# Kernel optimization log

Measured on AMD Instinct MI355X. Metric: run time of the kernel, lower is better.

Reference implementation:

```python
import jax, jax.numpy as jnp
import numpy as np
from jax import lax

DF = 64        # forcing_size: number of teacher-forced latent dims
TF_ALPHA = 0.2 # generalized teacher forcing interpolation weight


def setup_inputs() -> dict:
    key = jax.random.key(0)
    ks = jax.random.split(key, 8)
    B, T, dx, dz, dh, S = 256, 1024, 64, 256, 1024, 16
    x_gt = jax.random.normal(ks[0], (B, T, dx), dtype=jnp.float32)
    subject = jax.random.randint(ks[1], (B,), 0, S, dtype=jnp.int32)
    obs_matrix = jax.random.normal(ks[2], (dz, dx), dtype=jnp.float32) * 0.1
    A_table = jax.random.uniform(ks[3], (S, dz), dtype=jnp.float32) * 0.9
    W1_table = jax.random.normal(ks[4], (S, dz, dh), dtype=jnp.float32) * 0.02
    W2_table = jax.random.normal(ks[5], (S, dh, dz), dtype=jnp.float32) * 0.02
    h1_table = jax.random.normal(ks[6], (S, dz), dtype=jnp.float32) * 0.02
    h2_table = jax.random.normal(ks[7], (S, dh), dtype=jnp.float32) * 0.02
    return {"x_gt": x_gt, "subject": subject, "obs_matrix": obs_matrix,
            "A_table": A_table, "W1_table": W1_table, "W2_table": W2_table,
            "h1_table": h1_table, "h2_table": h2_table}


def reference(x_gt, subject, obs_matrix, A_table, W1_table, W2_table, h1_table, h2_table):
    B, T, dx = x_gt.shape
    dz = obs_matrix.shape[0]
    # encode: x @ pinv(obs_matrix) -> (B, T, dz)
    forcing = x_gt @ jnp.linalg.pinv(obs_matrix)
    # gather per-sample parameters by subject id
    A = A_table[subject]    # (B, dz)
    W1 = W1_table[subject]  # (B, dz, dh)
    W2 = W2_table[subject]  # (B, dh, dz)
    h1 = h1_table[subject]  # (B, dz)
    h2 = h2_table[subject]  # (B, dh)

    z0 = jnp.zeros((B, dz), dtype=x_gt.dtype)
    z0 = z0.at[:, :DF].set(forcing[:, 0, :DF])

    def step(z, f_t):
        # generalized teacher forcing on first DF dims
        z = z.at[:, :DF].set(TF_ALPHA * f_t[:, :DF] + (1.0 - TF_ALPHA) * z[:, :DF])
        # vanilla shPLRNN step: A*z + W1 @ relu(W2 @ z + h2) + h1
        hidden = jax.nn.relu(jnp.einsum('bhz,bz->bh', W2, z) + h2)
        z = A * z + jnp.einsum('bzh,bh->bz', W1, hidden) + h1
        return z, z

    _, Z = lax.scan(step, z0, jnp.transpose(forcing, (1, 0, 2)))  # Z: (T, B, dz)
    # decode: (B, T, dz) @ (dz, dx)
    return jnp.transpose(Z, (1, 0, 2)) @ obs_matrix
```

## Files before the change

kernel.cpp:

```cpp
#include <hip/hip_runtime.h>


typedef _Float16 f16;
typedef _Float16 f16x8 __attribute__((ext_vector_type(8)));
typedef float f32x4 __attribute__((ext_vector_type(4)));

#define TSTEPS 1024

#define WS_C     0ul
#define WS_ZG    16384ul
#define WS_HIDG  802816ul
#define WS_ORDER 2375680ul
#define WS_CNT   2376704ul
#define WS_OFFS  2376768ul
#define WS_CTR   2376832ul
#define WS_XCC   2378880ul
#define WS_NEED  2379392ul

#define SM_ZPK   0
#define SM_ZPRE  26880
#define SM_ZSL   33792
#define SM_TBUF  39936
#define SM_AH    53760
#define SM_ORD   54016
#define SM_SIZE  54208

__device__ __forceinline__ unsigned pack2f16(float x, float y) {
    union { f16 h[2]; unsigned u; } v;
    v.h[0] = (f16)x; v.h[1] = (f16)y;
    return v.u;
}

__device__ __forceinline__ void group_barrier(int* ctr, int target, bool light) {
    __syncthreads();
    if (threadIdx.x == 0) {
        if (!light)
            __builtin_amdgcn_fence(__ATOMIC_RELEASE, "agent");
        __hip_atomic_fetch_add(ctr, 1, __ATOMIC_RELAXED, __HIP_MEMORY_SCOPE_AGENT);
        while (__hip_atomic_load(ctr, __ATOMIC_RELAXED, __HIP_MEMORY_SCOPE_AGENT) < target)
            __builtin_amdgcn_s_sleep(1);
        if (!light)
            __builtin_amdgcn_fence(__ATOMIC_ACQUIRE, "agent");
        else
            asm volatile("buffer_inv" ::: "memory");
    }
    __syncthreads();
}

__global__ __launch_bounds__(256) void prep_kernel(const float* __restrict__ M,
                                                   float* __restrict__ C) {
    __shared__ float aug[64 * 132];
    __shared__ float fac[64];
    int tid = threadIdx.x;
    {
        int i = tid >> 2;
        int j0 = (tid & 3) * 16;
        float acc[16];
        #pragma unroll
        for (int e = 0; e < 16; ++e) acc[e] = 0.f;
        for (int r = 0; r < 256; ++r) {
            float mi = M[r*64 + i];
            #pragma unroll
            for (int e = 0; e < 16; ++e) acc[e] += mi * M[r*64 + j0 + e];
        }
        #pragma unroll
        for (int e = 0; e < 16; ++e) aug[i*132 + j0 + e] = acc[e];
    }
    for (int idx = tid; idx < 4096; idx += 256) {
        int x = idx >> 6, c = idx & 63;
        aug[x*132 + 64 + c] = M[c*64 + x];
    }
    __syncthreads();
    for (int p = 0; p < 64; ++p) {
        float piv = aug[p*132 + p];
        __syncthreads();
        if (tid < 128) aug[p*132 + tid] /= piv;
        __syncthreads();
        if (tid < 64) fac[tid] = aug[tid*132 + p];
        __syncthreads();
        for (int idx = tid; idx < 8192; idx += 256) {
            int r = idx >> 7, c = idx & 127;
            if (r != p) aug[r*132 + c] -= fac[r] * aug[p*132 + c];
        }
        __syncthreads();
    }
    for (int idx = tid; idx < 4096; idx += 256) {
        int x = idx >> 6, c = idx & 63;
        C[x*64 + c] = aug[x*132 + 64 + c];
    }
}

__global__ __launch_bounds__(256) void forcing_kernel(const float* __restrict__ x,
        const float* __restrict__ C, float* __restrict__ fout) {
    __shared__ float xs[64 * 68];
    __shared__ float Cs[64 * 64];
    int tid = threadIdx.x;
    for (int i = tid; i < 1024; i += 256)
        ((float4*)Cs)[i] = ((const float4*)C)[i];
    long r0 = (long)blockIdx.x * 64;
    int b  = (int)(r0 >> 10);
    int t0 = (int)(r0 & 1023);
    const float4* xb = (const float4*)(x + ((long)b * 1024 + t0) * 64);
    for (int i = tid; i < 1024; i += 256) {
        float4 v = xb[i];
        int row = i >> 4, col = (i & 15) * 4;
        *(float4*)&xs[row*68 + col] = v;
    }
    __syncthreads();
    int row = tid >> 2, cg = (tid & 3) * 16;
    float acc[16];
    #pragma unroll
    for (int e = 0; e < 16; ++e) acc[e] = 0.f;
    for (int k = 0; k < 64; ++k) {
        float xv = xs[row*68 + k];
        const float* cr = &Cs[k*64 + cg];
        #pragma unroll
        for (int e = 0; e < 16; ++e) acc[e] += xv * cr[e];
    }
    float4* dst = (float4*)(fout + ((size_t)b*1024 + t0 + row)*64 + cg);
    #pragma unroll
    for (int e = 0; e < 4; ++e) {
        float4 v; v.x = acc[4*e]; v.y = acc[4*e+1]; v.z = acc[4*e+2]; v.w = acc[4*e+3];
        dst[e] = v;
    }
}

__global__ __launch_bounds__(256) void group_kernel(const int* __restrict__ subject,
        int* order, int* cnt, int* offs, int* ctr) {
    __shared__ int lc[16], lo[16], cur[16];
    int tid = threadIdx.x;
    if (tid < 16) { lc[tid] = 0; cur[tid] = 0; }
    __syncthreads();
    int s = subject[tid];
    atomicAdd(&lc[s], 1);
    __syncthreads();
    if (tid == 0) { int a = 0; for (int i = 0; i < 16; ++i) { lo[i] = a; a += lc[i]; } }
    __syncthreads();
    int pos = lo[s] + atomicAdd(&cur[s], 1);
    order[pos] = tid;
    if (tid < 16) {
        cnt[tid] = lc[tid]; offs[tid] = lo[tid];
        ctr[tid*32] = 0;
        ctr[tid*32 + 16] = 0;
    }
}

template<int NT>
__device__ __forceinline__ void run_group(int s, int j, int Bs, int off,
    const float* __restrict__ W1t, const float* __restrict__ W2t,
    const float* __restrict__ At,  const float* __restrict__ h1t,
    const float* __restrict__ h2t, const float* __restrict__ Mt,
    float* __restrict__ zg, f16* __restrict__ hidg,
    const int* __restrict__ order, int* ctr, float* out, char* sm, bool light)
{
    f16*   zpk   = (f16*)(sm + SM_ZPK);
    f16*   zpre  = (f16*)(sm + SM_ZPRE);
    float* zsl   = (float*)(sm + SM_ZSL);
    f16*   tbuf  = (f16*)(sm + SM_TBUF);
    float* ah    = (float*)(sm + SM_AH);
    int*   ordl  = (int*)(sm + SM_ORD);
    float* red   = (float*)(sm + SM_ZPK);

    const int tid  = threadIdx.x;
    const int w    = tid >> 6;
    const int lane = tid & 63;
    const int q    = lane >> 4;
    const int li   = lane & 15;

    float* zgs = zg + (size_t)s * (48*256);
    char*  hgs = (char*)hidg + (size_t)s * (48*1024*2);

    if (tid < 48) ordl[tid] = (tid < Bs) ? order[off + tid] : 0;
    if (tid >= 64 && tid < 96)  ah[tid-64]      = At [s*256 + 32*j + (tid-64)];
    if (tid >= 96 && tid < 128) ah[tid-96+32]   = h1t[s*256 + 32*j + (tid-96)];
    __syncthreads();

    f16x8 w2f[2][8], w1f[2][8], mfr[8];
    float h2v[2][4];
    const f32x4 zero4 = {0.f, 0.f, 0.f, 0.f};
    #pragma unroll
    for (int m = 0; m < 2; ++m) {
        const float* src = W2t + (size_t)s*262144 + (size_t)(128*j + (2*w+m)*16 + li)*256;
        #pragma unroll
        for (int kt = 0; kt < 8; ++kt) {
            int k0 = kt*32 + q*8;
            #pragma unroll
            for (int e = 0; e < 8; ++e) w2f[m][kt][e] = (f16)src[k0+e];
        }
    }
    #pragma unroll
    for (int m = 0; m < 2; ++m) {
        const float* src = W1t + (size_t)s*262144 + (size_t)(32*j + m*16 + li)*1024;
        #pragma unroll
        for (int kt = 0; kt < 8; ++kt) {
            int k0 = (8*w + kt)*32 + q*8;
            #pragma unroll
            for (int e = 0; e < 8; ++e) w1f[m][kt][e] = (f16)src[k0+e];
        }
    }
    #pragma unroll
    for (int kt = 0; kt < 8; ++kt)
        #pragma unroll
        for (int e = 0; e < 8; ++e)
            mfr[kt][e] = (f16)Mt[(kt*32 + q*8 + e)*64 + 16*w + li];
    #pragma unroll
    for (int m = 0; m < 2; ++m)
        #pragma unroll
        for (int r = 0; r < 4; ++r)
            h2v[m][r] = h2t[s*1024 + 128*j + (2*w+m)*16 + q*4 + r];

    for (int idx = tid; idx < NT*512; idx += 256) {
        int n = idx >> 5, zdl = idx & 31;
        int zd = 32*j + zdl;
        float v = 0.f;
        if (zd < 64 && n < Bs) v = out[(size_t)ordl[n]*65536 + zd];
        zgs[n*256 + zd] = v;
    }
    int gen = 1;
    group_barrier(ctr, 8*gen, light);

    for (int t = 0; t <= TSTEPS; ++t) {
        {
            int half = tid >> 7;
            int kk = (tid & 127) * 2;
            int kl = kk - 32*j;
            #pragma unroll
            for (int i = 0; i < NT*8; ++i) {
                int n = i*2 + half;
                float zx = 0.f, zy = 0.f;
                if (n < Bs) {
                    float2 zz = *(const float2*)&zgs[n*256 + kk];
                    zx = zz.x; zy = zz.y;
                }
                float px = zx, py = zy;
                if (kk < 64) {
                    ((unsigned*)zpre)[n*36 + (kk>>1)] = pack2f16(zx, zy);
                    if (t < TSTEPS && n < Bs) {
                        float2 fv = *(const float2*)&out[((size_t)ordl[n]*1024 + t)*64 + kk];
                        px = 0.2f*fv.x + 0.8f*zx;
                        py = 0.2f*fv.y + 0.8f*zy;
                    }
                }
                ((unsigned*)zpk)[n*140 + (kk>>1)] = pack2f16(px, py);
                if (kl >= 0 && kl < 32) {
                    float2 pv; pv.x = px; pv.y = py;
                    *(float2*)&zsl[n*32 + kl] = pv;
                }
            }
        }
        __syncthreads();

        if (t > 0 && j < NT) {
            f32x4 dacc = zero4;
            #pragma unroll
            for (int kt = 0; kt < 8; ++kt) {
                f16x8 af;
                if (kt < 2) af = *(const f16x8*)&zpre[(16*j + li)*72 + kt*32 + q*8];
                else        af = *(const f16x8*)&zpk [(16*j + li)*280 + kt*32 + q*8];
                dacc = __builtin_amdgcn_mfma_f32_16x16x32_f16(af, mfr[kt], dacc, 0, 0, 0);
            }
            #pragma unroll
            for (int r = 0; r < 4; ++r) {
                int n = 16*j + q*4 + r;
                if (n < Bs)
                    out[((size_t)ordl[n]*TSTEPS + (t-1))*64 + 16*w + li] = dacc[r];
            }
        }
        if (t == TSTEPS) break;

        {
            f32x4 acc[2][NT];
            #pragma unroll
            for (int m = 0; m < 2; ++m)
                #pragma unroll
                for (int nt = 0; nt < NT; ++nt) acc[m][nt] = zero4;
            #pragma unroll
            for (int nt = 0; nt < NT; ++nt) {
                #pragma unroll
                for (int kt = 0; kt < 8; ++kt) {
                    f16x8 bf = *(const f16x8*)&zpk[(16*nt + li)*280 + kt*32 + q*8];
                    acc[0][nt] = __builtin_amdgcn_mfma_f32_16x16x32_f16(w2f[0][kt], bf, acc[0][nt], 0,0,0);
                    acc[1][nt] = __builtin_amdgcn_mfma_f32_16x16x32_f16(w2f[1][kt], bf, acc[1][nt], 0,0,0);
                }
            }
            #pragma unroll
            for (int m = 0; m < 2; ++m)
                #pragma unroll
                for (int nt = 0; nt < NT; ++nt)
                    #pragma unroll
                    for (int r = 0; r < 4; ++r) {
                        float hv = acc[m][nt][r] + h2v[m][r];
                        hv = hv > 0.f ? hv : 0.f;
                        tbuf[(nt*16 + li)*144 + (2*w+m)*16 + q*4 + r] = (f16)hv;
                    }
        }
        __syncthreads();
        for (int c = tid; c < NT*256; c += 256) {
            int n = c >> 4, cc = c & 15;
            *(f16x8*)(hgs + n*2048 + j*256 + cc*16) = *(const f16x8*)&tbuf[n*144 + cc*8];
        }
        ++gen; group_barrier(ctr, 8*gen, light);

        {
            f32x4 bacc[2][NT];
            #pragma unroll
            for (int m = 0; m < 2; ++m)
                #pragma unroll
                for (int nt = 0; nt < NT; ++nt) bacc[m][nt] = zero4;
            #pragma unroll
            for (int nt = 0; nt < NT; ++nt) {
                #pragma unroll
                for (int kt = 0; kt < 8; ++kt) {
                    f16x8 bf = *(const f16x8*)(hgs + (16*nt + li)*2048 + (8*w + kt)*64 + q*16);
                    bacc[0][nt] = __builtin_amdgcn_mfma_f32_16x16x32_f16(w1f[0][kt], bf, bacc[0][nt], 0,0,0);
                    bacc[1][nt] = __builtin_amdgcn_mfma_f32_16x16x32_f16(w1f[1][kt], bf, bacc[1][nt], 0,0,0);
                }
            }
            __syncthreads();
            #pragma unroll
            for (int m = 0; m < 2; ++m)
                #pragma unroll
                for (int nt = 0; nt < NT; ++nt)
                    *(f32x4*)&red[(size_t)((w*6 + m*3 + nt)*256 + lane*4)] = bacc[m][nt];
        }
        __syncthreads();
        for (int idx = tid; idx < NT*512; idx += 256) {
            int zdl = idx & 31, n = idx >> 5;
            int m = zdl >> 4, qq = (zdl >> 2) & 3, r = zdl & 3;
            int ln = qq*16 + (n & 15), nt = n >> 4;
            float sum = 0.f;
            #pragma unroll
            for (int ww = 0; ww < 4; ++ww)
                sum += red[(ww*6 + m*3 + nt)*256 + ln*4 + r];
            float zv = ah[zdl] * zsl[n*32 + zdl] + sum + ah[32 + zdl];
            if (n < Bs) zgs[n*256 + 32*j + zdl] = zv;
        }
        ++gen; group_barrier(ctr, 8*gen, light);
    }
}

__global__ __launch_bounds__(256, 1) void main_kernel(
    const float* W1t, const float* W2t, const float* At, const float* h1t,
    const float* h2t, const float* Mt, float* zg, f16* hidg,
    const int* order, const int* cnt, const int* offs, int* ctr, int* xccg,
    float* out)
{
    __shared__ __align__(16) char sm[SM_SIZE];
    int bid = blockIdx.x;
    int s = (bid & 7) + 8*(bid >> 6);
    int j = (bid >> 3) & 7;
    int Bs = cnt[s];
    if (Bs <= 0) return;
    if (Bs > 48) Bs = 48;
    int off = offs[s];
    int* myctr = ctr + s*32;

    int xcc;
    asm volatile("s_getreg_b32 %0, hwreg(HW_REG_XCC_ID)" : "=s"(xcc));
    xcc &= 0xf;
    if (threadIdx.x == 0) xccg[s*8 + j] = xcc;
    group_barrier(myctr + 16, 8, false);
    bool light = true;
    #pragma unroll
    for (int i = 0; i < 8; ++i) light = light && (xccg[s*8 + i] == xcc);

    int NT = (Bs + 15) >> 4;
    if (NT == 1)
        run_group<1>(s, j, Bs, off, W1t, W2t, At, h1t, h2t, Mt, zg, hidg, order, myctr, out, sm, light);
    else if (NT == 2)
        run_group<2>(s, j, Bs, off, W1t, W2t, At, h1t, h2t, Mt, zg, hidg, order, myctr, out, sm, light);
    else
        run_group<3>(s, j, Bs, off, W1t, W2t, At, h1t, h2t, Mt, zg, hidg, order, myctr, out, sm, light);
}

extern "C" void kernel_launch(void* const* d_in, const int* in_sizes, int n_in,
                              void* d_out, int out_size, void* d_ws, size_t ws_size,
                              hipStream_t stream) {
    const float* x    = (const float*)d_in[0];
    const int*   subj = (const int*)d_in[1];
    const float* Mt   = (const float*)d_in[2];
    const float* At   = (const float*)d_in[3];
    const float* W1t  = (const float*)d_in[4];
    const float* W2t  = (const float*)d_in[5];
    const float* h1t  = (const float*)d_in[6];
    const float* h2t  = (const float*)d_in[7];
    float* out = (float*)d_out;
    char*  ws  = (char*)d_ws;
    if (ws_size < WS_NEED) return;

    float* C     = (float*)(ws + WS_C);
    float* zg    = (float*)(ws + WS_ZG);
    f16*   hidg  = (f16*)(ws + WS_HIDG);
    int*   order = (int*)(ws + WS_ORDER);
    int*   cnt   = (int*)(ws + WS_CNT);
    int*   offs  = (int*)(ws + WS_OFFS);
    int*   ctr   = (int*)(ws + WS_CTR);
    int*   xccg  = (int*)(ws + WS_XCC);

    prep_kernel<<<1, 256, 0, stream>>>(Mt, C);
    forcing_kernel<<<4096, 256, 0, stream>>>(x, C, out);
    group_kernel<<<1, 256, 0, stream>>>(subj, order, cnt, offs, ctr);
    main_kernel<<<128, 256, 0, stream>>>(W1t, W2t, At, h1t, h2t, Mt,
                                         zg, hidg, order, cnt, offs, ctr, xccg, out);
}
```

Measured before the change: 10.94 ms.

## Split hidden dim across 4 blocks per subject with one barrier per step

Each subject group now uses 4 blocks instead of 8. Each block owns a 256-wide slice of the hidden dimension and computes W2 over the full z and its partial W1 product locally. The partial z contributions go to a double-buffered global scratch and are reduced redundantly by every block after a single group barrier per timestep, replacing the two barriers and the global hidden exchange of the old scheme. This halves cross-block synchronisation and uses fewer CUs, at the cost of twice the weights in registers per block, more MFMA work per block and redundant reduction reads.

```diff
diff --git a/kernel.cpp b/kernel.cpp
--- a/kernel.cpp
+++ b/kernel.cpp
@@ -8,28 +8,19 @@
 #define TSTEPS 1024
 
 #define WS_C     0ul
-#define WS_ZG    16384ul
-#define WS_HIDG  802816ul
-#define WS_ORDER 2375680ul
-#define WS_CNT   2376704ul
-#define WS_OFFS  2376768ul
-#define WS_CTR   2376832ul
-#define WS_XCC   2378880ul
-#define WS_NEED  2379392ul
+#define WS_P     16384ul
+#define WS_ORDER 6307840ul
+#define WS_CNT   6308864ul
+#define WS_OFFS  6308928ul
+#define WS_CTR   6308992ul
+#define WS_XCC   6311040ul
+#define WS_NEED  6311296ul
 
 #define SM_ZPK   0
 #define SM_ZPRE  26880
-#define SM_ZSL   33792
-#define SM_TBUF  39936
-#define SM_AH    53760
-#define SM_ORD   54016
-#define SM_SIZE  54208
-
-__device__ __forceinline__ unsigned pack2f16(float x, float y) {
-    union { f16 h[2]; unsigned u; } v;
-    v.h[0] = (f16)x; v.h[1] = (f16)y;
-    return v.u;
-}
+#define SM_TBUF  33792
+#define SM_ORD   60672
+#define SM_SIZE  60864
 
 __device__ __forceinline__ void group_barrier(int* ctr, int target, bool light) {
     __syncthreads();
@@ -150,37 +141,33 @@
     const float* __restrict__ W1t, const float* __restrict__ W2t,
     const float* __restrict__ At,  const float* __restrict__ h1t,
     const float* __restrict__ h2t, const float* __restrict__ Mt,
-    float* __restrict__ zg, f16* __restrict__ hidg,
-    const int* __restrict__ order, int* ctr, float* out, char* sm, bool light)
+    float* __restrict__ Pbuf, const int* __restrict__ order,
+    int* ctr, float* out, char* sm, bool light)
 {
-    f16*   zpk   = (f16*)(sm + SM_ZPK);
-    f16*   zpre  = (f16*)(sm + SM_ZPRE);
-    float* zsl   = (float*)(sm + SM_ZSL);
-    f16*   tbuf  = (f16*)(sm + SM_TBUF);
-    float* ah    = (float*)(sm + SM_AH);
-    int*   ordl  = (int*)(sm + SM_ORD);
-    float* red   = (float*)(sm + SM_ZPK);
+    f16*   zpk  = (f16*)(sm + SM_ZPK);
+    f16*   zpre = (f16*)(sm + SM_ZPRE);
+    f16*   tbuf = (f16*)(sm + SM_TBUF);
+    int*   ordl = (int*)(sm + SM_ORD);
 
     const int tid  = threadIdx.x;
     const int w    = tid >> 6;
     const int lane = tid & 63;
     const int q    = lane >> 4;
     const int li   = lane & 15;
-
-    float* zgs = zg + (size_t)s * (48*256);
-    char*  hgs = (char*)hidg + (size_t)s * (48*1024*2);
+    const int d    = tid;
 
     if (tid < 48) ordl[tid] = (tid < Bs) ? order[off + tid] : 0;
-    if (tid >= 64 && tid < 96)  ah[tid-64]      = At [s*256 + 32*j + (tid-64)];
-    if (tid >= 96 && tid < 128) ah[tid-96+32]   = h1t[s*256 + 32*j + (tid-96)];
-    __syncthreads();
-
-    f16x8 w2f[2][8], w1f[2][8], mfr[8];
-    float h2v[2][4];
+    __syncthreads();
+
+    const float an  = At [s*256 + d];
+    const float h1n = h1t[s*256 + d];
+
+    f16x8 w2f[4][8], w1f[4][8], mfr[8];
+    float h2v[4][4];
     const f32x4 zero4 = {0.f, 0.f, 0.f, 0.f};
     #pragma unroll
-    for (int m = 0; m < 2; ++m) {
-        const float* src = W2t + (size_t)s*262144 + (size_t)(128*j + (2*w+m)*16 + li)*256;
+    for (int m = 0; m < 4; ++m) {
+        const float* src = W2t + (size_t)s*262144 + (size_t)(256*j + 64*w + 16*m + li)*256;
         #pragma unroll
         for (int kt = 0; kt < 8; ++kt) {
             int k0 = kt*32 + q*8;
@@ -189,11 +176,11 @@
         }
     }
     #pragma unroll
-    for (int m = 0; m < 2; ++m) {
-        const float* src = W1t + (size_t)s*262144 + (size_t)(32*j + m*16 + li)*1024;
+    for (int m = 0; m < 4; ++m) {
+        const float* src = W1t + (size_t)s*262144 + (size_t)(64*w + 16*m + li)*1024 + 256*j;
         #pragma unroll
         for (int kt = 0; kt < 8; ++kt) {
-            int k0 = (8*w + kt)*32 + q*8;
+            int k0 = kt*32 + q*8;
             #pragma unroll
             for (int e = 0; e < 8; ++e) w1f[m][kt][e] = (f16)src[k0+e];
         }
@@ -204,51 +191,60 @@
         for (int e = 0; e < 8; ++e)
             mfr[kt][e] = (f16)Mt[(kt*32 + q*8 + e)*64 + 16*w + li];
     #pragma unroll
-    for (int m = 0; m < 2; ++m)
+    for (int m = 0; m < 4; ++m)
         #pragma unroll
         for (int r = 0; r < 4; ++r)
-            h2v[m][r] = h2t[s*1024 + 128*j + (2*w+m)*16 + q*4 + r];
-
-    for (int idx = tid; idx < NT*512; idx += 256) {
-        int n = idx >> 5, zdl = idx & 31;
-        int zd = 32*j + zdl;
-        float v = 0.f;
-        if (zd < 64 && n < Bs) v = out[(size_t)ordl[n]*65536 + zd];
-        zgs[n*256 + zd] = v;
-    }
-    int gen = 1;
-    group_barrier(ctr, 8*gen, light);
-
-    for (int t = 0; t <= TSTEPS; ++t) {
-        {
-            int half = tid >> 7;
-            int kk = (tid & 127) * 2;
-            int kl = kk - 32*j;
-            #pragma unroll
-            for (int i = 0; i < NT*8; ++i) {
-                int n = i*2 + half;
-                float zx = 0.f, zy = 0.f;
-                if (n < Bs) {
-                    float2 zz = *(const float2*)&zgs[n*256 + kk];
-                    zx = zz.x; zy = zz.y;
+            h2v[m][r] = h2t[s*1024 + 256*j + 64*w + 16*m + q*4 + r];
+
+    float azh[NT*16];
+    #pragma unroll
+    for (int n = 0; n < NT*16; ++n) {
+        float z0 = 0.f;
+        if (d < 64 && n < Bs) z0 = out[(size_t)ordl[n]*65536 + d];
+        zpk[n*280 + d] = (f16)z0;
+        if (d < 64) zpre[n*72 + d] = (f16)z0;
+        azh[n] = an*z0 + h1n;
+    }
+    __syncthreads();
+
+    int gen = 0;
+    for (int t = 0; t < TSTEPS; ++t) {
+        #pragma unroll
+        for (int nt = 0; nt < NT; ++nt) {
+            f32x4 acc[4] = {zero4, zero4, zero4, zero4};
+            #pragma unroll
+            for (int kt = 0; kt < 8; ++kt) {
+                f16x8 bf = *(const f16x8*)&zpk[(16*nt + li)*280 + kt*32 + q*8];
+                #pragma unroll
+                for (int m = 0; m < 4; ++m)
+                    acc[m] = __builtin_amdgcn_mfma_f32_16x16x32_f16(w2f[m][kt], bf, acc[m], 0,0,0);
+            }
+            #pragma unroll
+            for (int m = 0; m < 4; ++m)
+                #pragma unroll
+                for (int r = 0; r < 4; ++r) {
+                    float hv = acc[m][r] + h2v[m][r];
+                    hv = hv > 0.f ? hv : 0.f;
+                    tbuf[(16*nt + li)*280 + 64*w + 16*m + 4*q + r] = (f16)hv;
                 }
-                float px = zx, py = zy;
-                if (kk < 64) {
-                    ((unsigned*)zpre)[n*36 + (kk>>1)] = pack2f16(zx, zy);
-                    if (t < TSTEPS && n < Bs) {
-                        float2 fv = *(const float2*)&out[((size_t)ordl[n]*1024 + t)*64 + kk];
-                        px = 0.2f*fv.x + 0.8f*zx;
-                        py = 0.2f*fv.y + 0.8f*zy;
-                    }
-                }
-                ((unsigned*)zpk)[n*140 + (kk>>1)] = pack2f16(px, py);
-                if (kl >= 0 && kl < 32) {
-                    float2 pv; pv.x = px; pv.y = py;
-                    *(float2*)&zsl[n*32 + kl] = pv;
-                }
-            }
-        }
-        __syncthreads();
+        }
+        __syncthreads();
+
+        float* Pmy = Pbuf + (size_t)(((t & 1)*16 + s)*4 + j)*12288;
+        #pragma unroll
+        for (int nt = 0; nt < NT; ++nt) {
+            f32x4 bacc[4] = {zero4, zero4, zero4, zero4};
+            #pragma unroll
+            for (int kt = 0; kt < 8; ++kt) {
+                f16x8 bf = *(const f16x8*)&tbuf[(16*nt + li)*280 + kt*32 + q*8];
+                #pragma unroll
+                for (int m = 0; m < 4; ++m)
+                    bacc[m] = __builtin_amdgcn_mfma_f32_16x16x32_f16(w1f[m][kt], bf, bacc[m], 0,0,0);
+            }
+            #pragma unroll
+            for (int m = 0; m < 4; ++m)
+                *(f32x4*)&Pmy[(16*nt + li)*256 + 64*w + 16*m + 4*q] = bacc[m];
+        }
 
         if (t > 0 && j < NT) {
             f32x4 dacc = zero4;
@@ -266,89 +262,64 @@
                     out[((size_t)ordl[n]*TSTEPS + (t-1))*64 + 16*w + li] = dacc[r];
             }
         }
-        if (t == TSTEPS) break;
+
+        ++gen;
+        group_barrier(ctr, 4*gen, light);
 
         {
-            f32x4 acc[2][NT];
-            #pragma unroll
-            for (int m = 0; m < 2; ++m)
-                #pragma unroll
-                for (int nt = 0; nt < NT; ++nt) acc[m][nt] = zero4;
-            #pragma unroll
-            for (int nt = 0; nt < NT; ++nt) {
-                #pragma unroll
-                for (int kt = 0; kt < 8; ++kt) {
-                    f16x8 bf = *(const f16x8*)&zpk[(16*nt + li)*280 + kt*32 + q*8];
-                    acc[0][nt] = __builtin_amdgcn_mfma_f32_16x16x32_f16(w2f[0][kt], bf, acc[0][nt], 0,0,0);
-                    acc[1][nt] = __builtin_amdgcn_mfma_f32_16x16x32_f16(w2f[1][kt], bf, acc[1][nt], 0,0,0);
+            const float* Pb = Pbuf + (size_t)(((t & 1)*16 + s)*4)*12288;
+            const float* P0 = Pb;
+            const float* P1 = Pb + 12288;
+            const float* P2 = Pb + 24576;
+            const float* P3 = Pb + 36864;
+            #pragma unroll
+            for (int n = 0; n < NT*16; ++n) {
+                int o = n*256 + d;
+                float sum = (P0[o] + P1[o]) + (P2[o] + P3[o]);
+                float zr = azh[n] + sum;
+                float zh = zr;
+                if (d < 64) {
+                    zpre[n*72 + d] = (f16)zr;
+                    if (t+1 < TSTEPS && n < Bs) {
+                        float fv = out[(size_t)ordl[n]*65536 + (size_t)(t+1)*64 + d];
+                        zh = 0.2f*fv + 0.8f*zr;
+                    }
                 }
-            }
-            #pragma unroll
-            for (int m = 0; m < 2; ++m)
-                #pragma unroll
-                for (int nt = 0; nt < NT; ++nt)
-                    #pragma unroll
-                    for (int r = 0; r < 4; ++r) {
-                        float hv = acc[m][nt][r] + h2v[m][r];
-                        hv = hv > 0.f ? hv : 0.f;
-                        tbuf[(nt*16 + li)*144 + (2*w+m)*16 + q*4 + r] = (f16)hv;
-                    }
-        }
-        __syncthreads();
-        for (int c = tid; c < NT*256; c += 256) {
-            int n = c >> 4, cc = c & 15;
-            *(f16x8*)(hgs + n*2048 + j*256 + cc*16) = *(const f16x8*)&tbuf[n*144 + cc*8];
-        }
-        ++gen; group_barrier(ctr, 8*gen, light);
-
-        {
-            f32x4 bacc[2][NT];
-            #pragma unroll
-            for (int m = 0; m < 2; ++m)
-                #pragma unroll
-                for (int nt = 0; nt < NT; ++nt) bacc[m][nt] = zero4;
-            #pragma unroll
-            for (int nt = 0; nt < NT; ++nt) {
-                #pragma unroll
-                for (int kt = 0; kt < 8; ++kt) {
-                    f16x8 bf = *(const f16x8*)(hgs + (16*nt + li)*2048 + (8*w + kt)*64 + q*16);
-                    bacc[0][nt] = __builtin_amdgcn_mfma_f32_16x16x32_f16(w1f[0][kt], bf, bacc[0][nt], 0,0,0);
-                    bacc[1][nt] = __builtin_amdgcn_mfma_f32_16x16x32_f16(w1f[1][kt], bf, bacc[1][nt], 0,0,0);
-                }
-            }
-            __syncthreads();
-            #pragma unroll
-            for (int m = 0; m < 2; ++m)
-                #pragma unroll
-                for (int nt = 0; nt < NT; ++nt)
-                    *(f32x4*)&red[(size_t)((w*6 + m*3 + nt)*256 + lane*4)] = bacc[m][nt];
-        }
-        __syncthreads();
-        for (int idx = tid; idx < NT*512; idx += 256) {
-            int zdl = idx & 31, n = idx >> 5;
-            int m = zdl >> 4, qq = (zdl >> 2) & 3, r = zdl & 3;
-            int ln = qq*16 + (n & 15), nt = n >> 4;
-            float sum = 0.f;
-            #pragma unroll
-            for (int ww = 0; ww < 4; ++ww)
-                sum += red[(ww*6 + m*3 + nt)*256 + ln*4 + r];
-            float zv = ah[zdl] * zsl[n*32 + zdl] + sum + ah[32 + zdl];
-            if (n < Bs) zgs[n*256 + 32*j + zdl] = zv;
-        }
-        ++gen; group_barrier(ctr, 8*gen, light);
+                zpk[n*280 + d] = (f16)zh;
+                azh[n] = an*zh + h1n;
+            }
+        }
+        __syncthreads();
+    }
+
+    if (j < NT) {
+        f32x4 dacc = zero4;
+        #pragma unroll
+        for (int kt = 0; kt < 8; ++kt) {
+            f16x8 af;
+            if (kt < 2) af = *(const f16x8*)&zpre[(16*j + li)*72 + kt*32 + q*8];
+            else        af = *(const f16x8*)&zpk [(16*j + li)*280 + kt*32 + q*8];
+            dacc = __builtin_amdgcn_mfma_f32_16x16x32_f16(af, mfr[kt], dacc, 0, 0, 0);
+        }
+        #pragma unroll
+        for (int r = 0; r < 4; ++r) {
+            int n = 16*j + q*4 + r;
+            if (n < Bs)
+                out[((size_t)ordl[n]*TSTEPS + (TSTEPS-1))*64 + 16*w + li] = dacc[r];
+        }
     }
 }
 
 __global__ __launch_bounds__(256, 1) void main_kernel(
     const float* W1t, const float* W2t, const float* At, const float* h1t,
-    const float* h2t, const float* Mt, float* zg, f16* hidg,
+    const float* h2t, const float* Mt, float* Pbuf,
     const int* order, const int* cnt, const int* offs, int* ctr, int* xccg,
     float* out)
 {
     __shared__ __align__(16) char sm[SM_SIZE];
     int bid = blockIdx.x;
-    int s = (bid & 7) + 8*(bid >> 6);
-    int j = (bid >> 3) & 7;
+    int s = bid & 15;
+    int j = bid >> 4;
     int Bs = cnt[s];
     if (Bs <= 0) return;
     if (Bs > 48) Bs = 48;
@@ -358,19 +329,19 @@
     int xcc;
     asm volatile("s_getreg_b32 %0, hwreg(HW_REG_XCC_ID)" : "=s"(xcc));
     xcc &= 0xf;
-    if (threadIdx.x == 0) xccg[s*8 + j] = xcc;
-    group_barrier(myctr + 16, 8, false);
+    if (threadIdx.x == 0) xccg[s*4 + j] = xcc;
+    group_barrier(myctr + 16, 4, false);
     bool light = true;
     #pragma unroll
-    for (int i = 0; i < 8; ++i) light = light && (xccg[s*8 + i] == xcc);
+    for (int i = 0; i < 4; ++i) light = light && (xccg[s*4 + i] == xcc);
 
     int NT = (Bs + 15) >> 4;
     if (NT == 1)
-        run_group<1>(s, j, Bs, off, W1t, W2t, At, h1t, h2t, Mt, zg, hidg, order, myctr, out, sm, light);
+        run_group<1>(s, j, Bs, off, W1t, W2t, At, h1t, h2t, Mt, Pbuf, order, myctr, out, sm, light);
     else if (NT == 2)
-        run_group<2>(s, j, Bs, off, W1t, W2t, At, h1t, h2t, Mt, zg, hidg, order, myctr, out, sm, light);
+        run_group<2>(s, j, Bs, off, W1t, W2t, At, h1t, h2t, Mt, Pbuf, order, myctr, out, sm, light);
     else
-        run_group<3>(s, j, Bs, off, W1t, W2t, At, h1t, h2t, Mt, zg, hidg, order, myctr, out, sm, light);
+        run_group<3>(s, j, Bs, off, W1t, W2t, At, h1t, h2t, Mt, Pbuf, order, myctr, out, sm, light);
 }
 
 extern "C" void kernel_launch(void* const* d_in, const int* in_sizes, int n_in,
@@ -389,8 +360,7 @@
     if (ws_size < WS_NEED) return;
 
     float* C     = (float*)(ws + WS_C);
-    float* zg    = (float*)(ws + WS_ZG);
-    f16*   hidg  = (f16*)(ws + WS_HIDG);
+    float* Pbuf  = (float*)(ws + WS_P);
     int*   order = (int*)(ws + WS_ORDER);
     int*   cnt   = (int*)(ws + WS_CNT);
     int*   offs  = (int*)(ws + WS_OFFS);
@@ -400,6 +370,6 @@
     prep_kernel<<<1, 256, 0, stream>>>(Mt, C);
     forcing_kernel<<<4096, 256, 0, stream>>>(x, C, out);
     group_kernel<<<1, 256, 0, stream>>>(subj, order, cnt, offs, ctr);
-    main_kernel<<<128, 256, 0, stream>>>(W1t, W2t, At, h1t, h2t, Mt,
-                                         zg, hidg, order, cnt, offs, ctr, xccg, out);
-}
+    main_kernel<<<64, 256, 0, stream>>>(W1t, W2t, At, h1t, h2t, Mt,
+                                        Pbuf, order, cnt, offs, ctr, xccg, out);
+}
```

After: 16.19 ms. 1.48x slower.
